# Performance work log

Hardware: AMD Instinct MI355X
Metric: run time of the kernel (lower is better)

Reference implementation:

```python
import jax, jax.numpy as jnp
import numpy as np

B, S, D = 8, 1024, 768
H, DK, DV = 12, 64, 64


def setup_inputs() -> dict:
    key = jax.random.key(0)
    ks = jax.random.split(key, 8)
    s_in = 1.0 / np.sqrt(D)
    s_cat = 1.0 / np.sqrt(H * DV)
    return {
        "x": jax.random.normal(ks[0], (B, S, D), jnp.float32),
        "Wq": jax.random.normal(ks[1], (H, D, DK), jnp.float32) * s_in,
        "bq": jnp.zeros((H, DK), jnp.float32),
        "Wk": jax.random.normal(ks[2], (H, D, DK), jnp.float32) * s_in,
        "bk": jnp.zeros((H, DK), jnp.float32),
        "Wv": jax.random.normal(ks[3], (H, D, DV), jnp.float32) * s_in,
        "bv": jnp.zeros((H, DV), jnp.float32),
        "W0": jax.random.normal(ks[4], (H * DV, D), jnp.float32) * s_cat,
        "b0": jnp.zeros((D,), jnp.float32),
    }


def reference(x, Wq, bq, Wk, bk, Wv, bv, W0, b0):
    # Per-head projections, batched across heads (same math as the ModuleList loop).
    q = jnp.einsum("bsd,hdk->bhsk", x, Wq) + bq[None, :, None, :]  # [B,H,S,DK]
    k = jnp.einsum("bsd,hdk->bhsk", x, Wk) + bk[None, :, None, :]
    v = jnp.einsum("bsd,hdv->bhsv", x, Wv) + bv[None, :, None, :]
    scale = 1.0 / jnp.sqrt(jnp.asarray(DK, x.dtype))
    scores = jnp.einsum("bhqk,bhsk->bhqs", q, k) * scale  # [B,H,S,S]
    causal = jnp.tril(jnp.ones((S, S), bool))
    scores = jnp.where(causal[None, None], scores, jnp.asarray(-1e9, x.dtype))
    attn = jax.nn.softmax(scores, axis=-1)
    out = jnp.einsum("bhqs,bhsv->bhqv", attn, v)  # [B,H,S,DV]
    # concat heads along last dim -> [B,S,H*DV]
    out = jnp.transpose(out, (0, 2, 1, 3)).reshape(B, S, H * DV)
    # output projection (dropout is identity in eval mode / p=0)
    return out @ W0 + b0
```

## Files before the change

kernel.cpp:

```cpp
#include <hip/hip_runtime.h>


typedef __attribute__((ext_vector_type(8))) short short8;
typedef __attribute__((ext_vector_type(4))) short short4_t;
typedef __attribute__((ext_vector_type(4))) float f32x4;

#define Bsz 8
#define Ssz 1024
#define Dsz 768
#define Hsz 12
#define DKsz 64
#define KVB 128

__device__ __forceinline__ short f2bf(float f) {
    unsigned u = __float_as_uint(f);
    u = (u + 0x7fffu + ((u >> 16) & 1u)) >> 16;
    return (short)u;
}

__device__ __forceinline__ float fexp2(float x) {
    float r;
    asm("v_exp_f32 %0, %1" : "=v"(r) : "v"(x));
    return r;
}

__device__ __forceinline__ f32x4 mfma16(short8 a, short8 b, f32x4 c) {
    return __builtin_amdgcn_mfma_f32_16x16x32_bf16(a, b, c, 0, 0, 0);
}

__device__ __forceinline__ void gload16(const short* g, short* lds) {
    __builtin_amdgcn_global_load_lds(
        (const __attribute__((address_space(1))) void*)g,
        (__attribute__((address_space(3))) void*)lds, 16, 0, 0);
}

template <int N> __device__ __forceinline__ void waitv() {
    if constexpr (N == 4)      asm volatile("s_waitcnt vmcnt(4)" ::: "memory");
    else if constexpr (N == 3) asm volatile("s_waitcnt vmcnt(3)" ::: "memory");
    else                       asm volatile("s_waitcnt vmcnt(0)" ::: "memory");
}

__global__ __launch_bounds__(256) void cast_x_kernel(const float* __restrict__ x,
                                                     short* __restrict__ xbf) {
    int i = (blockIdx.x * 256 + threadIdx.x) * 8;
    float4 a = *reinterpret_cast<const float4*>(&x[i]);
    float4 b = *reinterpret_cast<const float4*>(&x[i + 4]);
    short8 o;
    o[0] = f2bf(a.x); o[1] = f2bf(a.y); o[2] = f2bf(a.z); o[3] = f2bf(a.w);
    o[4] = f2bf(b.x); o[5] = f2bf(b.y); o[6] = f2bf(b.z); o[7] = f2bf(b.w);
    *reinterpret_cast<short8*>(&xbf[i]) = o;
}

__global__ __launch_bounds__(256) void pack_qkvw_kernel(const float* __restrict__ Wq,
                                                        const float* __restrict__ Wk,
                                                        const float* __restrict__ Wv,
                                                        short* __restrict__ Wt) {
    int idx = blockIdx.x * 256 + threadIdx.x;
    int n = idx / Dsz;
    int k = idx % Dsz;
    int which = n / 768;
    int hc = n - which * 768;
    int h = hc >> 6, c = hc & 63;
    const float* W = (which == 0) ? Wq : (which == 1) ? Wk : Wv;
    Wt[idx] = f2bf(W[(h * Dsz + k) * DKsz + c]);
}

__global__ __launch_bounds__(256) void pack_w0_kernel(const float* __restrict__ W0,
                                                      short* __restrict__ W0t) {
    int idx = blockIdx.x * 256 + threadIdx.x;
    int n = idx / Dsz;
    int k = idx % Dsz;
    W0t[idx] = f2bf(W0[k * Dsz + n]);
}

#define GEMM_MAIN256(A_, Bt_, Kdim, NF_, WAITN_)                                   \
    int tid = threadIdx.x, w = tid >> 6, l = tid & 63;                             \
    int wr = w >> 2, wc = w & 3;                                                   \
    int lr = l & 15, lg = l >> 4;                                                  \
    __shared__ short Als[2][256 * 32];                                             \
    __shared__ short Bls[2][(NF_ * 64) * 32];                                      \
    f32x4 acc[8][NF_] = {};                                                        \
    auto STAGE = [&](int cb, int k0) {                                             \
        _Pragma("unroll")                                                          \
        for (int it = 0; it < 2; ++it) {                                           \
            int i = it * 512 + tid;                                                \
            int r = i >> 2, sl = i & 3;                                            \
            gload16((A_) + r * (Kdim) + k0 + ((sl ^ (r & 3)) << 3),                \
                    &Als[cb][(it * 512 + w * 64) * 8]);                            \
        }                                                                          \
        _Pragma("unroll")                                                          \
        for (int it = 0; it < (NF_) / 2; ++it) {                                   \
            int i = it * 512 + tid;                                                \
            int r = i >> 2, sl = i & 3;                                            \
            gload16((Bt_) + r * (Kdim) + k0 + ((sl ^ (r & 3)) << 3),               \
                    &Bls[cb][(it * 512 + w * 64) * 8]);                            \
        }                                                                          \
    };                                                                             \
    auto COMPUTE = [&](int cb) {                                                   \
        short8 bf[NF_];                                                            \
        _Pragma("unroll")                                                          \
        for (int n = 0; n < (NF_); ++n) {                                          \
            int row = wc * ((NF_) * 16) + n * 16 + lr;                             \
            bf[n] = *reinterpret_cast<const short8*>(                              \
                &Bls[cb][row * 32 + ((lg ^ (row & 3)) << 3)]);                     \
        }                                                                          \
        _Pragma("unroll")                                                          \
        for (int m = 0; m < 8; ++m) {                                              \
            int row = wr * 128 + m * 16 + lr;                                      \
            short8 af = *reinterpret_cast<const short8*>(                          \
                &Als[cb][row * 32 + ((lg ^ (row & 3)) << 3)]);                     \
            _Pragma("unroll")                                                      \
            for (int n = 0; n < (NF_); ++n)                                        \
                acc[m][n] = mfma16(af, bf[n], acc[m][n]);                          \
        }                                                                          \
    };                                                                             \
    STAGE(0, 0);                                                                   \
    STAGE(1, 32);                                                                  \
    for (int k = 0; k < (Kdim) / 32 - 2; ++k) {                                    \
        waitv<WAITN_>();                                                           \
        __builtin_amdgcn_s_barrier();                                              \
        COMPUTE(k & 1);                                                            \
        __builtin_amdgcn_s_barrier();                                              \
        STAGE(k & 1, (k + 2) * 32);                                                \
    }                                                                              \
    waitv<WAITN_>();                                                               \
    __builtin_amdgcn_s_barrier();                                                  \
    COMPUTE(((Kdim) / 32 - 2) & 1);                                                \
    waitv<0>();                                                                    \
    __builtin_amdgcn_s_barrier();                                                  \
    COMPUTE(((Kdim) / 32 - 1) & 1);

__global__ __launch_bounds__(512, 2) void gemm_qkv_kernel(
    const short* __restrict__ A, const short* __restrict__ Bt,
    const float* __restrict__ bq, const float* __restrict__ bk,
    const float* __restrict__ bv,
    short* __restrict__ Qb, short* __restrict__ Kb, short* __restrict__ Vb) {
    int tile = (blockIdx.x & 7) * 36 + (blockIdx.x >> 3);
    int tm = tile / 9, tn = tile % 9;
    const short* Ab = A + (size_t)tm * 256 * Dsz;
    const short* Bb = Bt + (size_t)tn * 256 * Dsz;
    GEMM_MAIN256(Ab, Bb, Dsz, 4, 4)
    int which = tn / 3;
    const float* bias = (which == 0) ? bq : (which == 1) ? bk : bv;
    int row0 = tm * 256 + wr * 128;
    int col0 = tn * 256 + wc * 64 - which * 768;
    if (which == 2) {
#pragma unroll
        for (int m = 0; m < 8; ++m)
#pragma unroll
            for (int n = 0; n < 4; ++n) {
                int s0 = row0 + m * 16 + lg * 4;
                int col = col0 + n * 16 + lr;
                int b = s0 >> 10, s = s0 & 1023;
                int h = col >> 6, c = col & 63;
                float bi = bias[h * 64 + c];
                short4_t pk;
#pragma unroll
                for (int j = 0; j < 4; ++j) pk[j] = f2bf(acc[m][n][j] + bi);
                *reinterpret_cast<short4_t*>(
                    &Vb[(((size_t)b * Hsz + h) * DKsz + c) * Ssz + s]) = pk;
            }
    } else {
        short* dst = (which == 0) ? Qb : Kb;
#pragma unroll
        for (int m = 0; m < 8; ++m)
#pragma unroll
            for (int n = 0; n < 4; ++n)
#pragma unroll
                for (int j = 0; j < 4; ++j) {
                    int row = row0 + m * 16 + lg * 4 + j;
                    int col = col0 + n * 16 + lr;
                    int b = row >> 10, s = row & 1023;
                    int h = col >> 6, c = col & 63;
                    float v = acc[m][n][j] + bias[h * 64 + c];
                    if (which == 0) v *= 0.180336884f;
                    dst[(((size_t)b * Hsz + h) * Ssz + s) * DKsz + c] = f2bf(v);
                }
    }
}

__global__ __launch_bounds__(256) void attn_kernel(const short* __restrict__ Q,
                                                   const short* __restrict__ K,
                                                   const short* __restrict__ Vt,
                                                   short* __restrict__ O) {
    int raw = blockIdx.x;
    int xcd = raw & 7, slot = raw >> 3;
    int bh  = (slot >> 4) * 8 + xcd;
    int qb  = 15 - (slot & 15);
    const short* Qh = Q + (size_t)bh * Ssz * DKsz;
    const short* Kh = K + (size_t)bh * Ssz * DKsz;
    const short* Vh = Vt + (size_t)bh * DKsz * Ssz;
    int tid = threadIdx.x, w = tid >> 6, l = tid & 63;
    int lr = l & 15, lg = l >> 4;
    __shared__ short Kls[KVB * 64];
    __shared__ short Vls[64 * KVB];
    __shared__ short Pls[4][16 * KVB];

    int qrow = qb * 64 + w * 16 + lr;
    short8 aq0 = *reinterpret_cast<const short8*>(&Qh[qrow * 64 + lg * 8]);
    short8 aq1 = *reinterpret_cast<const short8*>(&Qh[qrow * 64 + 32 + lg * 8]);

    short8 ones;
#pragma unroll
    for (int e = 0; e < 8; ++e) ones[e] = (short)0x3F80;

    f32x4 acc[4] = {};
    f32x4 accL = {};

    int nt = qb / 2 + 1;
    for (int t = 0; t < nt; ++t) {
        __syncthreads();
        const short* Ksrc = Kh + t * KVB * 64;
#pragma unroll
        for (int it = 0; it < 4; ++it) {
            int i = it * 256 + tid;
            int r = i >> 3, ps = i & 7;
            gload16(Ksrc + r * 64 + ((ps ^ (r & 7)) << 3),
                    &Kls[(it * 256 + w * 64) * 8]);
        }
#pragma unroll
        for (int it = 0; it < 4; ++it) {
            int i = it * 256 + tid;
            int r = i >> 4, ps = i & 15;
            gload16(Vh + r * Ssz + t * KVB + ((ps ^ (r & 15)) << 3),
                    &Vls[(it * 256 + w * 64) * 8]);
        }
        __syncthreads();

        f32x4 s[8] = {};
        __builtin_amdgcn_s_setprio(1);
#pragma unroll
        for (int n = 0; n < 8; ++n) {
            int kr = n * 16 + lr;
            short8 kf0 = *reinterpret_cast<const short8*>(
                &Kls[kr * 64 + ((lg ^ (kr & 7)) << 3)]);
            short8 kf1 = *reinterpret_cast<const short8*>(
                &Kls[kr * 64 + (((lg + 4) ^ (kr & 7)) << 3)]);
            s[n] = mfma16(aq0, kf0, s[n]);
            s[n] = mfma16(aq1, kf1, s[n]);
        }
        __builtin_amdgcn_s_setprio(0);

        if (t == nt - 1) {
#pragma unroll
            for (int n = 0; n < 8; ++n)
#pragma unroll
                for (int j = 0; j < 4; ++j) {
                    int kv = t * KVB + n * 16 + lr;
                    int q = qb * 64 + w * 16 + lg * 4 + j;
                    if (kv > q) s[n][j] = -1e30f;
                }
        }

#pragma unroll
        for (int n = 0; n < 8; ++n)
#pragma unroll
            for (int j = 0; j < 4; ++j) {
                float p = fexp2(s[n][j]);
                int row = lg * 4 + j;
                int col = n * 16 + lr;
                Pls[w][row * KVB + (col ^ (row << 3))] = f2bf(p);
            }

        __builtin_amdgcn_s_setprio(1);
#pragma unroll
        for (int kk = 0; kk < 4; ++kk) {
            int sl = (((kk * 4 + lg) ^ lr) << 3);
            short8 pa = *reinterpret_cast<const short8*>(&Pls[w][lr * KVB + sl]);
            accL = mfma16(pa, ones, accL);
#pragma unroll
            for (int n = 0; n < 4; ++n) {
                short8 vf = *reinterpret_cast<const short8*>(
                    &Vls[(n * 16 + lr) * KVB + sl]);
                acc[n] = mfma16(pa, vf, acc[n]);
            }
        }
        __builtin_amdgcn_s_setprio(0);
    }

    int b = bh / Hsz, h = bh % Hsz;
#pragma unroll
    for (int n = 0; n < 4; ++n)
#pragma unroll
        for (int j = 0; j < 4; ++j) {
            int q = qb * 64 + w * 16 + lg * 4 + j;
            int dv = n * 16 + lr;
            float o = acc[n][j] / accL[j];
            O[((size_t)(b * Ssz + q)) * Dsz + h * DKsz + dv] = f2bf(o);
        }
}

__global__ __launch_bounds__(512, 2) void gemm_out_kernel(const short* __restrict__ A,
                                                          const short* __restrict__ Bt,
                                                          const float* __restrict__ b0,
                                                          float* __restrict__ out) {
    int tile = (blockIdx.x & 7) * 24 + (blockIdx.x >> 3);
    int tm = tile / 6, tn = tile % 6;
    const short* Ab = A + (size_t)tm * 256 * Dsz;
    const short* Bb = Bt + (size_t)tn * 128 * Dsz;
    GEMM_MAIN256(Ab, Bb, Dsz, 2, 3)
    int row0 = tm * 256 + wr * 128;
    int col0 = tn * 128 + wc * 32;
#pragma unroll
    for (int m = 0; m < 8; ++m)
#pragma unroll
        for (int n = 0; n < 2; ++n)
#pragma unroll
            for (int j = 0; j < 4; ++j) {
                int row = row0 + m * 16 + lg * 4 + j;
                int col = col0 + n * 16 + lr;
                out[(size_t)row * Dsz + col] = acc[m][n][j] + b0[col];
            }
}

extern "C" void kernel_launch(void* const* d_in, const int* in_sizes, int n_in,
                              void* d_out, int out_size, void* d_ws, size_t ws_size,
                              hipStream_t stream) {
    const float* x  = (const float*)d_in[0];
    const float* Wq = (const float*)d_in[1];
    const float* bq = (const float*)d_in[2];
    const float* Wk = (const float*)d_in[3];
    const float* bk = (const float*)d_in[4];
    const float* Wv = (const float*)d_in[5];
    const float* bv = (const float*)d_in[6];
    const float* W0 = (const float*)d_in[7];
    const float* b0 = (const float*)d_in[8];
    float* out = (float*)d_out;

    const size_t N_X   = (size_t)Bsz * Ssz * Dsz;
    const size_t N_QKV = (size_t)3 * Dsz * Dsz;
    const size_t N_W0  = (size_t)Dsz * Dsz;
    const size_t N_HD  = (size_t)Bsz * Hsz * Ssz * DKsz;

    short* xbf   = (short*)d_ws;
    short* wqkvt = xbf + N_X;
    short* w0t   = wqkvt + N_QKV;
    short* Qb    = w0t + N_W0;
    short* Kb    = Qb + N_HD;
    short* Vb    = Kb + N_HD;
    short* attno = Vb + N_HD;

    cast_x_kernel<<<(int)(N_X / 2048), 256, 0, stream>>>(x, xbf);
    pack_qkvw_kernel<<<(int)(N_QKV / 256), 256, 0, stream>>>(Wq, Wk, Wv, wqkvt);
    pack_w0_kernel<<<(int)(N_W0 / 256), 256, 0, stream>>>(W0, w0t);
    gemm_qkv_kernel<<<288, 512, 0, stream>>>(xbf, wqkvt, bq, bk, bv, Qb, Kb, Vb);
    attn_kernel<<<Bsz * Hsz * 16, 256, 0, stream>>>(Qb, Kb, Vb, attno);
    gemm_out_kernel<<<192, 512, 0, stream>>>(attno, w0t, b0, out);
}
```

Before: 226.5 us.

## Triple-buffer GEMM LDS stages and double-buffer K/V tiles in attention

The GEMM main loop moves to a three-stage LDS ring. Each iteration now issues the next-but-one load before computing, so one barrier per k-step is removed. The LDS swizzle is changed to XOR with (row>>1)&3, which is meant to reduce bank conflicts for the 32-wide rows. The attention kernel double-buffers its K/V tiles and prefetches the next tile while computing the current one, waiting with a vmcnt of 8 instead of a full sync. The extra LDS per block may reduce occupancy, and the GEMM callers must now pass wait counts that match the new load schedule.

```diff
diff --git a/kernel.cpp b/kernel.cpp
--- a/kernel.cpp
+++ b/kernel.cpp
@@ -35,7 +35,8 @@
 }
 
 template <int N> __device__ __forceinline__ void waitv() {
-    if constexpr (N == 4)      asm volatile("s_waitcnt vmcnt(4)" ::: "memory");
+    if constexpr (N == 8)      asm volatile("s_waitcnt vmcnt(8)" ::: "memory");
+    else if constexpr (N == 4) asm volatile("s_waitcnt vmcnt(4)" ::: "memory");
     else if constexpr (N == 3) asm volatile("s_waitcnt vmcnt(3)" ::: "memory");
     else                       asm volatile("s_waitcnt vmcnt(0)" ::: "memory");
 }
@@ -73,26 +74,26 @@
     W0t[idx] = f2bf(W0[k * Dsz + n]);
 }
 
-#define GEMM_MAIN256(A_, Bt_, Kdim, NF_, WAITN_)                                   \
+#define GEMM_MAIN256(A_, Bt_, Kdim, NF_, WAITL_)                                   \
     int tid = threadIdx.x, w = tid >> 6, l = tid & 63;                             \
     int wr = w >> 2, wc = w & 3;                                                   \
     int lr = l & 15, lg = l >> 4;                                                  \
-    __shared__ short Als[2][256 * 32];                                             \
-    __shared__ short Bls[2][(NF_ * 64) * 32];                                      \
+    __shared__ short Als[3][256 * 32];                                             \
+    __shared__ short Bls[3][(NF_ * 64) * 32];                                      \
     f32x4 acc[8][NF_] = {};                                                        \
     auto STAGE = [&](int cb, int k0) {                                             \
         _Pragma("unroll")                                                          \
         for (int it = 0; it < 2; ++it) {                                           \
             int i = it * 512 + tid;                                                \
             int r = i >> 2, sl = i & 3;                                            \
-            gload16((A_) + r * (Kdim) + k0 + ((sl ^ (r & 3)) << 3),                \
+            gload16((A_) + r * (Kdim) + k0 + ((sl ^ ((r >> 1) & 3)) << 3),         \
                     &Als[cb][(it * 512 + w * 64) * 8]);                            \
         }                                                                          \
         _Pragma("unroll")                                                          \
         for (int it = 0; it < (NF_) / 2; ++it) {                                   \
             int i = it * 512 + tid;                                                \
             int r = i >> 2, sl = i & 3;                                            \
-            gload16((Bt_) + r * (Kdim) + k0 + ((sl ^ (r & 3)) << 3),               \
+            gload16((Bt_) + r * (Kdim) + k0 + ((sl ^ ((r >> 1) & 3)) << 3),        \
                     &Bls[cb][(it * 512 + w * 64) * 8]);                            \
         }                                                                          \
     };                                                                             \
@@ -102,33 +103,30 @@
         for (int n = 0; n < (NF_); ++n) {                                          \
             int row = wc * ((NF_) * 16) + n * 16 + lr;                             \
             bf[n] = *reinterpret_cast<const short8*>(                              \
-                &Bls[cb][row * 32 + ((lg ^ (row & 3)) << 3)]);                     \
+                &Bls[cb][row * 32 + ((lg ^ ((row >> 1) & 3)) << 3)]);              \
         }                                                                          \
         _Pragma("unroll")                                                          \
         for (int m = 0; m < 8; ++m) {                                              \
             int row = wr * 128 + m * 16 + lr;                                      \
             short8 af = *reinterpret_cast<const short8*>(                          \
-                &Als[cb][row * 32 + ((lg ^ (row & 3)) << 3)]);                     \
+                &Als[cb][row * 32 + ((lg ^ ((row >> 1) & 3)) << 3)]);              \
             _Pragma("unroll")                                                      \
             for (int n = 0; n < (NF_); ++n)                                        \
                 acc[m][n] = mfma16(af, bf[n], acc[m][n]);                          \
         }                                                                          \
     };                                                                             \
+    const int ns = (Kdim) / 32;                                                    \
     STAGE(0, 0);                                                                   \
     STAGE(1, 32);                                                                  \
-    for (int k = 0; k < (Kdim) / 32 - 2; ++k) {                                    \
-        waitv<WAITN_>();                                                           \
+    for (int k = 0; k < ns - 1; ++k) {                                             \
+        waitv<WAITL_>();                                                           \
         __builtin_amdgcn_s_barrier();                                              \
-        COMPUTE(k & 1);                                                            \
-        __builtin_amdgcn_s_barrier();                                              \
-        STAGE(k & 1, (k + 2) * 32);                                                \
+        if (k + 2 < ns) STAGE((k + 2) % 3, (k + 2) * 32);                          \
+        COMPUTE(k % 3);                                                            \
     }                                                                              \
-    waitv<WAITN_>();                                                               \
-    __builtin_amdgcn_s_barrier();                                                  \
-    COMPUTE(((Kdim) / 32 - 2) & 1);                                                \
     waitv<0>();                                                                    \
     __builtin_amdgcn_s_barrier();                                                  \
-    COMPUTE(((Kdim) / 32 - 1) & 1);
+    COMPUTE((ns - 1) % 3);
 
 __global__ __launch_bounds__(512, 2) void gemm_qkv_kernel(
     const short* __restrict__ A, const short* __restrict__ Bt,
@@ -192,40 +190,46 @@
     const short* Vh = Vt + (size_t)bh * DKsz * Ssz;
     int tid = threadIdx.x, w = tid >> 6, l = tid & 63;
     int lr = l & 15, lg = l >> 4;
-    __shared__ short Kls[KVB * 64];
-    __shared__ short Vls[64 * KVB];
+    __shared__ short Kls[2][KVB * 64];
+    __shared__ short Vls[2][64 * KVB];
     __shared__ short Pls[4][16 * KVB];
 
-    int qrow = qb * 64 + w * 16 + lr;
-    short8 aq0 = *reinterpret_cast<const short8*>(&Qh[qrow * 64 + lg * 8]);
-    short8 aq1 = *reinterpret_cast<const short8*>(&Qh[qrow * 64 + 32 + lg * 8]);
-
-    short8 ones;
-#pragma unroll
-    for (int e = 0; e < 8; ++e) ones[e] = (short)0x3F80;
-
-    f32x4 acc[4] = {};
-    f32x4 accL = {};
-
-    int nt = qb / 2 + 1;
-    for (int t = 0; t < nt; ++t) {
-        __syncthreads();
+    auto STAGEKV = [&](int cb, int t) {
         const short* Ksrc = Kh + t * KVB * 64;
 #pragma unroll
         for (int it = 0; it < 4; ++it) {
             int i = it * 256 + tid;
             int r = i >> 3, ps = i & 7;
             gload16(Ksrc + r * 64 + ((ps ^ (r & 7)) << 3),
-                    &Kls[(it * 256 + w * 64) * 8]);
+                    &Kls[cb][(it * 256 + w * 64) * 8]);
         }
 #pragma unroll
         for (int it = 0; it < 4; ++it) {
             int i = it * 256 + tid;
             int r = i >> 4, ps = i & 15;
             gload16(Vh + r * Ssz + t * KVB + ((ps ^ (r & 15)) << 3),
-                    &Vls[(it * 256 + w * 64) * 8]);
-        }
-        __syncthreads();
+                    &Vls[cb][(it * 256 + w * 64) * 8]);
+        }
+    };
+
+    int qrow = qb * 64 + w * 16 + lr;
+    short8 aq0 = *reinterpret_cast<const short8*>(&Qh[qrow * 64 + lg * 8]);
+    short8 aq1 = *reinterpret_cast<const short8*>(&Qh[qrow * 64 + 32 + lg * 8]);
+
+    short8 ones;
+#pragma unroll
+    for (int e = 0; e < 8; ++e) ones[e] = (short)0x3F80;
+
+    f32x4 acc[4] = {};
+    f32x4 accL = {};
+
+    int nt = qb / 2 + 1;
+    STAGEKV(0, 0);
+    for (int t = 0; t < nt; ++t) {
+        int cb = t & 1;
+        if (t + 1 < nt) { STAGEKV(cb ^ 1, t + 1); waitv<8>(); }
+        else            { waitv<0>(); }
+        __builtin_amdgcn_s_barrier();
 
         f32x4 s[8] = {};
         __builtin_amdgcn_s_setprio(1);
@@ -233,9 +237,9 @@
         for (int n = 0; n < 8; ++n) {
             int kr = n * 16 + lr;
             short8 kf0 = *reinterpret_cast<const short8*>(
-                &Kls[kr * 64 + ((lg ^ (kr & 7)) << 3)]);
+                &Kls[cb][kr * 64 + ((lg ^ (kr & 7)) << 3)]);
             short8 kf1 = *reinterpret_cast<const short8*>(
-                &Kls[kr * 64 + (((lg + 4) ^ (kr & 7)) << 3)]);
+                &Kls[cb][kr * 64 + (((lg + 4) ^ (kr & 7)) << 3)]);
             s[n] = mfma16(aq0, kf0, s[n]);
             s[n] = mfma16(aq1, kf1, s[n]);
         }
@@ -271,11 +275,12 @@
 #pragma unroll
             for (int n = 0; n < 4; ++n) {
                 short8 vf = *reinterpret_cast<const short8*>(
-                    &Vls[(n * 16 + lr) * KVB + sl]);
+                    &Vls[cb][(n * 16 + lr) * KVB + sl]);
                 acc[n] = mfma16(pa, vf, acc[n]);
             }
         }
         __builtin_amdgcn_s_setprio(0);
+        __builtin_amdgcn_s_barrier();
     }
 
     int b = bh / Hsz, h = bh % Hsz;
```

After: 243.4 us. 7.5% more time.
